# Kernel tuning notes

Hardware: AMD Instinct MI355X
Metric: run time of the kernel (lower is better)

Reference implementation:

```python
import jax, jax.numpy as jnp
import numpy as np

CL1_K = 25
CL2_K = 25


def cheb_stack(L, x0, K):
    # x0: (V, M) -> (K, V, M) Chebyshev basis T_k(L) x0
    if K == 1:
        return x0[None]
    x1 = L @ x0
    if K == 2:
        return jnp.stack([x0, x1])

    def step(carry, _):
        xm1, xm2 = carry
        xk = 2.0 * (L @ xm1) - xm2
        return (xk, xm1), xk

    _, rest = jax.lax.scan(step, (x1, x0), None, length=K - 2)
    return jnp.concatenate([x0[None], x1[None], rest], axis=0)


def graph_conv(x, L, W, b, K):
    # x: (B, C, V) -> (B, Fout, V); matches torch Graph_Conv permute/view logic
    B, C, V = x.shape
    x0 = x.transpose(2, 1, 0).reshape(V, C * B)
    xs = cheb_stack(L, x0, K)                              # (K, V, C*B)
    xs = xs.reshape(K, V, C, B).transpose(3, 1, 2, 0)      # (B, V, C, K)
    xs = xs.reshape(B * V, C * K)
    y = xs @ W.T + b                                       # (B*V, Fout)
    return y.reshape(B, V, -1).transpose(0, 2, 1)


def maxpool4(x):
    B, C, V = x.shape
    return x.reshape(B, C, V // 4, 4).max(axis=-1)


def setup_inputs() -> dict:
    key = jax.random.key(0)
    ks = jax.random.split(key, 10)
    B, C, V, Vp = 32, 16, 4000, 4096
    CL1_F, CL2_F, FC_F = 64, 128, 10
    x = jax.random.normal(ks[0], (B, C, V), dtype=jnp.float32)
    perm = jax.random.permutation(ks[1], Vp)
    # rescaled Laplacians, scaled for stable 25-step recurrence
    L1 = jax.random.normal(ks[2], (Vp, Vp), dtype=jnp.float32) * (0.3 / np.sqrt(Vp))
    L2 = jax.random.normal(ks[3], (Vp // 4, Vp // 4), dtype=jnp.float32) * (0.3 / np.sqrt(Vp // 4))
    W1 = jax.random.normal(ks[4], (CL1_F, C * CL1_K), dtype=jnp.float32) * np.sqrt(2.0 / (C * CL1_K + CL1_F))
    b1 = jnp.zeros((CL1_F,), dtype=jnp.float32)
    W2 = jax.random.normal(ks[5], (CL2_F, CL1_F * CL2_K), dtype=jnp.float32) * np.sqrt(2.0 / (CL1_F * CL2_K + CL2_F))
    b2 = jnp.zeros((CL2_F,), dtype=jnp.float32)
    FC_IN = CL2_F * Vp // 16
    Wfc = jax.random.normal(ks[6], (FC_F, FC_IN), dtype=jnp.float32) * np.sqrt(2.0 / (FC_IN + FC_F))
    bfc = jnp.zeros((FC_F,), dtype=jnp.float32)
    return {"x": x, "perm": perm, "L1": L1, "L2": L2, "W1": W1, "b1": b1,
            "W2": W2, "b2": b2, "Wfc": Wfc, "bfc": bfc}


def reference(x, perm, L1, L2, W1, b1, W2, b2, Wfc, bfc):
    # BatchNorm1d(affine=False), training-mode batch statistics
    mu = x.mean(axis=(0, 2), keepdims=True)
    var = x.var(axis=(0, 2), keepdims=True)
    x = (x - mu) / jnp.sqrt(var + 1e-5)
    # Permute: zero-pad vertices to len(perm), then index
    B, C, V = x.shape
    Vp = perm.shape[0]
    x = jnp.pad(x, ((0, 0), (0, 0), (0, Vp - V)))[:, :, perm]
    x = jax.nn.relu(graph_conv(x, L1, W1, b1, CL1_K))
    x = maxpool4(x)
    x = jax.nn.relu(graph_conv(x, L2, W2, b2, CL2_K))
    x = maxpool4(x)
    x = x.reshape(B, -1)
    # dropout in eval mode (identity)
    return x @ Wfc.T + bfc
```

## Files before the change

### kernel.cpp

```cpp
#include <hip/hip_runtime.h>

typedef _Float16 half8 __attribute__((ext_vector_type(8)));
typedef _Float16 half4 __attribute__((ext_vector_type(4)));
typedef float f32x4 __attribute__((ext_vector_type(4)));

__device__ __forceinline__ void gload_lds16(const void* g, void* l) {
  __builtin_amdgcn_global_load_lds((const __attribute__((address_space(1))) void*)g,
                                   (__attribute__((address_space(3))) void*)l, 16, 0, 0);
}

__global__ __launch_bounds__(256) void k_bn_partial(const float* __restrict__ x,
                                                    float* __restrict__ part) {
  const int c = blockIdx.x & 15;
  const int seg = blockIdx.x >> 4;
  const int t = threadIdx.x;
  float s = 0.f, s2 = 0.f;
  for (int b = 0; b < 32; ++b) {
    const float* row = x + (size_t)(b * 16 + c) * 4000 + seg * 500;
    for (int v = t; v < 500; v += 256) {
      float val = row[v];
      s += val;
      s2 += val * val;
    }
  }
#pragma unroll
  for (int off = 32; off > 0; off >>= 1) {
    s += __shfl_down(s, off);
    s2 += __shfl_down(s2, off);
  }
  __shared__ float rs_[4], rs2_[4];
  if ((t & 63) == 0) { rs_[t >> 6] = s; rs2_[t >> 6] = s2; }
  __syncthreads();
  if (t == 0) {
    part[c * 8 + seg] = rs_[0] + rs_[1] + rs_[2] + rs_[3];
    part[128 + c * 8 + seg] = rs2_[0] + rs2_[1] + rs2_[2] + rs2_[3];
  }
}

__global__ void k_bn_final(const float* __restrict__ part, float* __restrict__ musig) {
  const int c = threadIdx.x;
  if (c < 16) {
    float S = 0.f, S2 = 0.f;
#pragma unroll
    for (int seg = 0; seg < 8; ++seg) {
      S += part[c * 8 + seg];
      S2 += part[128 + c * 8 + seg];
    }
    const float inv = 1.f / 128000.f;
    float mu = S * inv;
    float var = S2 * inv - mu * mu;
    musig[c] = mu;
    musig[16 + c] = rsqrtf(var + 1e-5f);
  }
}

__global__ __launch_bounds__(256) void k_build_x0(const float* __restrict__ x,
                                                  const int* __restrict__ perm,
                                                  const float* __restrict__ musig,
                                                  _Float16* __restrict__ X0) {
  const int idx = blockIdx.x * 256 + threadIdx.x;
  const int v = idx & 4095;
  const int m = idx >> 12;
  const int b = m & 31;
  const int c = m >> 5;
  const int pv = perm[v];
  float val = 0.f;
  if (pv < 4000)
    val = (x[((size_t)(b * 16 + c)) * 4000 + pv] - musig[c]) * musig[16 + c] * 0.0625f;
  X0[idx] = (_Float16)val;
}

__global__ __launch_bounds__(256) void k_cvt_f16(const float* __restrict__ s,
                                                 _Float16* __restrict__ d, int n) {
  const int i = (blockIdx.x * 256 + threadIdx.x) * 4;
  if (i >= n) return;
  f32x4 v = *(const f32x4*)(s + i);
  half4 h;
  h[0] = (_Float16)v[0]; h[1] = (_Float16)v[1];
  h[2] = (_Float16)v[2]; h[3] = (_Float16)v[3];
  *(half4*)(d + i) = h;
}

__global__ __launch_bounds__(256) void k_prep_w(const float* __restrict__ W,
                                                _Float16* __restrict__ Wp,
                                                int F, int shiftC, int kround) {
  const int idx = blockIdx.x * 256 + threadIdx.x;
  const int CS = 1 << shiftC;
  const int KPtot = kround * CS;
  if (idx >= F * KPtot) return;
  const int f = idx / KPtot;
  const int rem = idx - f * KPtot;
  const int k = rem >> shiftC;
  const int c = rem & (CS - 1);
  float v = 0.f;
  if (k < 25) v = W[(size_t)f * (CS * 25) + c * 25 + k];
  Wp[idx] = (_Float16)v;
}

__global__ __launch_bounds__(512, 1) void k_cheb_ks(const _Float16* __restrict__ Xprev,
                                                    const _Float16* __restrict__ Lm,
                                                    _Float16* __restrict__ P) {
  __shared__ _Float16 lds[2][24576];
  const int t = threadIdx.x;
  const int lane = t & 63;
  const int w = t >> 6;
  const int wm = w >> 2, wn = w & 3;
  const int bid = blockIdx.x;
  const int bx = bid & 15;
  const int by = (bid >> 4) & 3;
  const int kq = bid >> 6;
  const int v0 = bx * 256, m0 = by * 128;
  const size_t rs = 8192;

  const char* Ag = (const char*)Xprev + (size_t)m0 * rs + (size_t)kq * 2048;
  const char* Bg = (const char*)Lm + (size_t)v0 * rs + (size_t)kq * 2048;
  const size_t soff = (size_t)(lane >> 3) * rs + (size_t)(((lane & 7) * 16) ^ ((lane >> 3) << 4));

  f32x4 acc[4][4] = {};

  auto stage = [&](int buf, int tt) {
    const char* ag = Ag + (size_t)tt * 128 + soff;
    const char* bg = Bg + (size_t)tt * 128 + soff;
    char* A = (char*)&lds[buf][0];
    char* B = (char*)&lds[buf][8192];
#pragma unroll
    for (int j = 0; j < 2; ++j) {
      const int r0 = w * 16 + j * 8;
      gload_lds16(ag + (size_t)r0 * rs, A + r0 * 128);
    }
#pragma unroll
    for (int j = 0; j < 4; ++j) {
      const int r0 = w * 32 + j * 8;
      gload_lds16(bg + (size_t)r0 * rs, B + r0 * 128);
    }
  };

  stage(0, 0);

  const int NT = 16;
  for (int tt = 0; tt < NT; ++tt) {
    const int cur = tt & 1;
    if (tt + 1 < NT) {
      stage(cur ^ 1, tt + 1);
      asm volatile("s_waitcnt vmcnt(6)" ::: "memory");
    } else {
      asm volatile("s_waitcnt vmcnt(0)" ::: "memory");
    }
    asm volatile("s_barrier" ::: "memory");
    const char* A = (const char*)&lds[cur][0];
    const char* B = (const char*)&lds[cur][8192];
#pragma unroll
    for (int kk = 0; kk < 2; ++kk) {
      const int cb = kk * 64 + ((lane >> 4) << 4);
      half8 a[4], b[4];
#pragma unroll
      for (int mi = 0; mi < 4; ++mi) {
        const int ar = wm * 64 + mi * 16 + (lane & 15);
        a[mi] = *(const half8*)(A + ar * 128 + (cb ^ ((ar & 7) << 4)));
      }
#pragma unroll
      for (int ni = 0; ni < 4; ++ni) {
        const int br = wn * 64 + ni * 16 + (lane & 15);
        b[ni] = *(const half8*)(B + br * 128 + (cb ^ ((br & 7) << 4)));
      }
#pragma unroll
      for (int mi = 0; mi < 4; ++mi)
#pragma unroll
        for (int ni = 0; ni < 4; ++ni)
          acc[mi][ni] = __builtin_amdgcn_mfma_f32_16x16x32_f16(a[mi], b[ni], acc[mi][ni], 0, 0, 0);
    }
    asm volatile("s_barrier" ::: "memory");
  }

  _Float16* Pq = P + (size_t)kq * 2097152;
  const int rbase = (lane >> 4) << 2;
#pragma unroll
  for (int mi = 0; mi < 4; ++mi) {
#pragma unroll
    for (int ni = 0; ni < 4; ++ni) {
      const int vv = v0 + wn * 64 + ni * 16 + (lane & 15);
#pragma unroll
      for (int r = 0; r < 4; ++r) {
        const int mm = m0 + wm * 64 + mi * 16 + rbase + r;
        Pq[(size_t)mm * 4096 + vv] = (_Float16)acc[mi][ni][r];
      }
    }
  }
}

__global__ __launch_bounds__(256) void k_cheb_red(const _Float16* __restrict__ P,
                                                  const _Float16* __restrict__ Xm2,
                                                  _Float16* __restrict__ Xout,
                                                  float alpha, float beta) {
  const int i = (blockIdx.x * 256 + threadIdx.x) * 8;
  half8 p0 = *(const half8*)(P + i);
  half8 p1 = *(const half8*)(P + 2097152 + i);
  half8 p2 = *(const half8*)(P + 4194304 + i);
  half8 p3 = *(const half8*)(P + 6291456 + i);
  half8 xm2 = {};
  if (beta != 0.f) xm2 = *(const half8*)(Xm2 + i);
  half8 o;
#pragma unroll
  for (int j = 0; j < 8; ++j) {
    float s = (float)p0[j] + (float)p1[j] + (float)p2[j] + (float)p3[j];
    o[j] = (_Float16)(alpha * s - beta * (float)xm2[j]);
  }
  *(half8*)(Xout + i) = o;
}

__global__ __launch_bounds__(512, 2) void k_cheb(const _Float16* __restrict__ Xprev,
                                                 const _Float16* __restrict__ Lm,
                                                 const _Float16* __restrict__ Xm2,
                                                 _Float16* __restrict__ Xout,
                                                 int V, float alpha, float beta) {
  __shared__ _Float16 lds[2][2][12288];
  const int t = threadIdx.x;
  const int lane = t & 63;
  const int w = t >> 6;
  const int kh = w >> 2;
  const int wl = w & 3;
  const int wr = wl >> 1, wc = wl & 1;
  const int v0 = blockIdx.x * 64;
  const int m0 = blockIdx.y * 128;
  const size_t rs = (size_t)V * 2;
  const int K2 = V >> 1;
  const int NT2 = K2 >> 6;

  const char* Ag = (const char*)Xprev + (size_t)m0 * rs + (size_t)kh * K2 * 2;
  const char* Bg = (const char*)Lm + (size_t)v0 * rs + (size_t)kh * K2 * 2;
  const size_t soff = (size_t)(lane >> 3) * rs + (size_t)(((lane & 7) * 16) ^ ((lane >> 3) << 4));

  f32x4 acc[4][2] = {};

  auto stage = [&](int buf, int tt) {
    const char* ag = Ag + (size_t)tt * 128 + soff;
    const char* bg = Bg + (size_t)tt * 128 + soff;
    char* A = (char*)&lds[kh][buf][0];
    char* B = (char*)&lds[kh][buf][8192];
#pragma unroll
    for (int j = 0; j < 4; ++j) {
      const int r0 = wl * 32 + j * 8;
      gload_lds16(ag + (size_t)r0 * rs, A + r0 * 128);
    }
#pragma unroll
    for (int j = 0; j < 2; ++j) {
      const int r0 = wl * 16 + j * 8;
      gload_lds16(bg + (size_t)r0 * rs, B + r0 * 128);
    }
  };

  stage(0, 0);

  for (int tt = 0; tt < NT2; ++tt) {
    const int cur = tt & 1;
    if (tt + 1 < NT2) {
      stage(cur ^ 1, tt + 1);
      asm volatile("s_waitcnt vmcnt(6)" ::: "memory");
    } else {
      asm volatile("s_waitcnt vmcnt(0)" ::: "memory");
    }
    asm volatile("s_barrier" ::: "memory");
    const char* A = (const char*)&lds[kh][cur][0];
    const char* B = (const char*)&lds[kh][cur][8192];
#pragma unroll
    for (int kk = 0; kk < 2; ++kk) {
      const int cb = kk * 64 + ((lane >> 4) << 4);
      half8 a[4], b[2];
#pragma unroll
      for (int mi = 0; mi < 4; ++mi) {
        const int ar = wr * 64 + mi * 16 + (lane & 15);
        a[mi] = *(const half8*)(A + ar * 128 + (cb ^ ((ar & 7) << 4)));
      }
#pragma unroll
      for (int ni = 0; ni < 2; ++ni) {
        const int br = wc * 32 + ni * 16 + (lane & 15);
        b[ni] = *(const half8*)(B + br * 128 + (cb ^ ((br & 7) << 4)));
      }
#pragma unroll
      for (int mi = 0; mi < 4; ++mi)
#pragma unroll
        for (int ni = 0; ni < 2; ++ni)
          acc[mi][ni] = __builtin_amdgcn_mfma_f32_16x16x32_f16(a[mi], b[ni], acc[mi][ni], 0, 0, 0);
    }
    asm volatile("s_barrier" ::: "memory");
  }

  __syncthreads();
  float* red = (float*)&lds[0][0][0];
  if (kh == 1) {
    float* dst = red + wl * 2048 + lane * 4;
#pragma unroll
    for (int mi = 0; mi < 4; ++mi)
#pragma unroll
      for (int ni = 0; ni < 2; ++ni)
        *(f32x4*)(dst + (mi * 2 + ni) * 256) = acc[mi][ni];
  }
  __syncthreads();
  if (kh == 0) {
    const float* src = red + wl * 2048 + lane * 4;
    const int rbase = (lane >> 4) << 2;
#pragma unroll
    for (int mi = 0; mi < 4; ++mi) {
#pragma unroll
      for (int ni = 0; ni < 2; ++ni) {
        f32x4 o = *(const f32x4*)(src + (mi * 2 + ni) * 256);
        const int vv = v0 + wc * 32 + ni * 16 + (lane & 15);
#pragma unroll
        for (int r = 0; r < 4; ++r) {
          const int mm = m0 + wr * 64 + mi * 16 + rbase + r;
          const size_t idx = (size_t)mm * V + vv;
          float val = alpha * (acc[mi][ni][r] + o[r]);
          if (beta != 0.f) val -= (float)Xm2[idx];
          Xout[idx] = (_Float16)val;
        }
      }
    }
  }
}

__global__ __launch_bounds__(256, 2) void k_dense(const _Float16* __restrict__ Wp,
                                                  const _Float16* __restrict__ XS,
                                                  const float* __restrict__ bias,
                                                  float* __restrict__ Yt,
                                                  int Vv, int shiftC, int nsteps,
                                                  size_t planeV, int Ntot,
                                                  float ascale, float bscale) {
  __shared__ _Float16 Alds[64 * 40];
  __shared__ _Float16 Blds[32 * 66];
  const int t = threadIdx.x;
  const int lane = t & 63;
  const int w = t >> 6;
  const int n0 = blockIdx.x * 64;
  const int f0 = blockIdx.y * 64;
  const int b = n0 / Vv;
  const int vb = n0 % Vv;
  const int KP = nsteps * 32;
  const int cmask = (1 << shiftC) - 1;

  f32x4 acc0 = {0.f, 0.f, 0.f, 0.f}, acc1 = {0.f, 0.f, 0.f, 0.f};
  f32x4 acc2 = {0.f, 0.f, 0.f, 0.f}, acc3 = {0.f, 0.f, 0.f, 0.f};

  for (int s = 0; s < nsteps; ++s) {
    const int q0 = s * 32;
    {
      const int row = t >> 2, cb = (t & 3) * 16;
      half8 v = *(const half8*)((const char*)Wp + ((size_t)(f0 + row) * KP + q0) * 2 + cb);
      *(half8*)((char*)Alds + row * 80 + cb) = v;
    }
    {
      const int q = q0 + (t >> 3), cb = (t & 7) * 16;
      const int k = q >> shiftC, c = q & cmask;
      half8 v = {};
      if (k < 25)
        v = *(const half8*)((const char*)XS +
                            ((size_t)k * planeV + (size_t)(c * 32 + b) * Vv + vb) * 2 + cb);
      uint4 uv = *(uint4*)&v;
      uint* ud = (uint*)((char*)Blds + (t >> 3) * 132 + cb);
      ud[0] = uv.x; ud[1] = uv.y; ud[2] = uv.z; ud[3] = uv.w;
    }
    __syncthreads();
    const int g16 = (lane >> 4) << 4;
    half8 a0 = *(const half8*)((char*)Alds + ((lane & 15) + 0) * 80 + g16);
    half8 a1 = *(const half8*)((char*)Alds + ((lane & 15) + 16) * 80 + g16);
    half8 a2 = *(const half8*)((char*)Alds + ((lane & 15) + 32) * 80 + g16);
    half8 a3 = *(const half8*)((char*)Alds + ((lane & 15) + 48) * 80 + g16);
    half8 bf;
    const int col = (w << 4) + (lane & 15);
#pragma unroll
    for (int j = 0; j < 8; ++j)
      bf[j] = Blds[(((lane >> 4) << 3) + j) * 66 + col];
    acc0 = __builtin_amdgcn_mfma_f32_16x16x32_f16(a0, bf, acc0, 0, 0, 0);
    acc1 = __builtin_amdgcn_mfma_f32_16x16x32_f16(a1, bf, acc1, 0, 0, 0);
    acc2 = __builtin_amdgcn_mfma_f32_16x16x32_f16(a2, bf, acc2, 0, 0, 0);
    acc3 = __builtin_amdgcn_mfma_f32_16x16x32_f16(a3, bf, acc3, 0, 0, 0);
    __syncthreads();
  }

  const int n = n0 + (w << 4) + (lane & 15);
  f32x4 accs[4] = {acc0, acc1, acc2, acc3};
#pragma unroll
  for (int mi = 0; mi < 4; ++mi) {
#pragma unroll
    for (int r = 0; r < 4; ++r) {
      const int f = f0 + (mi << 4) + ((lane >> 4) << 2) + r;
      float val = ascale * accs[mi][r] + bscale * bias[f];
      Yt[(size_t)f * Ntot + n] = fmaxf(val, 0.f);
    }
  }
}

__global__ __launch_bounds__(256) void k_pool1(const float* __restrict__ Yt,
                                               _Float16* __restrict__ X2) {
  const int idx = blockIdx.x * 256 + threadIdx.x;
  const int v2 = idx & 1023;
  const int rest = idx >> 10;
  const int b = rest & 31;
  const int f = rest >> 5;
  f32x4 q = *(const f32x4*)(Yt + (size_t)f * 131072 + b * 4096 + v2 * 4);
  float mx = fmaxf(fmaxf(q[0], q[1]), fmaxf(q[2], q[3]));
  X2[(size_t)(f * 32 + b) * 1024 + v2] = (_Float16)(mx * 0.015625f);
}

__global__ __launch_bounds__(256) void k_pool2(const float* __restrict__ Yt,
                                               float* __restrict__ p2) {
  const int idx = blockIdx.x * 256 + threadIdx.x;
  const int v3 = idx & 255;
  const int rest = idx >> 8;
  const int f = rest & 127;
  const int b = rest >> 7;
  f32x4 q = *(const f32x4*)(Yt + (size_t)f * 32768 + b * 1024 + v3 * 4);
  float mx = fmaxf(fmaxf(q[0], q[1]), fmaxf(q[2], q[3]));
  p2[(size_t)b * 32768 + f * 256 + v3] = mx;
}

__global__ __launch_bounds__(256) void k_fc_part(const float* __restrict__ p2,
                                                 const float* __restrict__ Wfc,
                                                 float* __restrict__ partF) {
  const int b = blockIdx.x >> 3;
  const int seg = blockIdx.x & 7;
  const int t = threadIdx.x;
  const int lane = t & 63;
  const int w = t >> 6;
  const int base = seg * 4096;
  float acc[10];
#pragma unroll
  for (int o = 0; o < 10; ++o) acc[o] = 0.f;
  const float* pb = p2 + (size_t)b * 32768 + base;
  for (int i = t; i < 4096; i += 256) {
    float p = pb[i];
#pragma unroll
    for (int o = 0; o < 10; ++o) acc[o] += p * Wfc[(size_t)o * 32768 + base + i];
  }
#pragma unroll
  for (int off = 32; off > 0; off >>= 1)
#pragma unroll
    for (int o = 0; o < 10; ++o) acc[o] += __shfl_down(acc[o], off);
  __shared__ float rws[10][4];
  if (lane == 0) {
#pragma unroll
    for (int o = 0; o < 10; ++o) rws[o][w] = acc[o];
  }
  __syncthreads();
  if (t < 10) partF[blockIdx.x * 10 + t] =
      rws[t][0] + rws[t][1] + rws[t][2] + rws[t][3];
}

__global__ void k_fc_final(const float* __restrict__ partF,
                           const float* __restrict__ bfc,
                           float* __restrict__ out) {
  const int t = threadIdx.x;
  if (t < 320) {
    const int b = t / 10, o = t - b * 10;
    float s = 0.f;
#pragma unroll
    for (int seg = 0; seg < 8; ++seg) s += partF[(b * 8 + seg) * 10 + o];
    out[b * 10 + o] = 64.f * s + bfc[o];
  }
}

extern "C" void kernel_launch(void* const* d_in, const int* in_sizes, int n_in,
                              void* d_out, int out_size, void* d_ws, size_t ws_size,
                              hipStream_t stream) {
  (void)in_sizes; (void)n_in; (void)out_size; (void)ws_size;
  const float* x = (const float*)d_in[0];
  const int* perm = (const int*)d_in[1];
  const float* L1 = (const float*)d_in[2];
  const float* L2 = (const float*)d_in[3];
  const float* W1 = (const float*)d_in[4];
  const float* b1 = (const float*)d_in[5];
  const float* W2 = (const float*)d_in[6];
  const float* b2 = (const float*)d_in[7];
  const float* Wfc = (const float*)d_in[8];
  const float* bfc = (const float*)d_in[9];
  float* out = (float*)d_out;

  char* ws = (char*)d_ws;
  size_t off = 0;
  auto alloc = [&](size_t bytes) {
    char* p = ws + off;
    off += (bytes + 255) & ~(size_t)255;
    return p;
  };
  _Float16* L1h = (_Float16*)alloc(16777216ull * 2);
  _Float16* L2h = (_Float16*)alloc(1048576ull * 2);
  _Float16* W1p = (_Float16*)alloc(64ull * 448 * 2);
  _Float16* W2p = (_Float16*)alloc(128ull * 1664 * 2);
  float* part = (float*)alloc(256 * 4);
  float* musig = (float*)alloc(32 * 4);
  float* partF = (float*)alloc(2560 * 4);
  _Float16* XS = (_Float16*)alloc(25ull * 2097152 * 2);
  _Float16* Pq = (_Float16*)alloc(4ull * 2097152 * 2);
  float* Yt = (float*)alloc(64ull * 131072 * 4);
  float* p2 = (float*)alloc(32ull * 128 * 256 * 4);

  k_cvt_f16<<<16384, 256, 0, stream>>>(L1, L1h, 16777216);
  k_cvt_f16<<<1024, 256, 0, stream>>>(L2, L2h, 1048576);
  k_prep_w<<<112, 256, 0, stream>>>(W1, W1p, 64, 4, 28);
  k_prep_w<<<832, 256, 0, stream>>>(W2, W2p, 128, 6, 26);
  k_bn_partial<<<128, 256, 0, stream>>>(x, part);
  k_bn_final<<<1, 64, 0, stream>>>(part, musig);
  k_build_x0<<<8192, 256, 0, stream>>>(x, perm, musig, XS);

  const size_t plane = 2097152;
  for (int k = 1; k < 25; ++k) {
    k_cheb_ks<<<256, 512, 0, stream>>>(XS + (size_t)(k - 1) * plane, L1h, Pq);
    k_cheb_red<<<1024, 256, 0, stream>>>(
        Pq, XS + (size_t)(k >= 2 ? k - 2 : 0) * plane, XS + (size_t)k * plane,
        (k == 1) ? 1.f : 2.f, (k == 1) ? 0.f : 1.f);
  }
  k_dense<<<dim3(2048, 1), 256, 0, stream>>>(W1p, XS, b1, Yt, 4096, 4, 14, plane,
                                             131072, 16.f, 1.f);
  k_pool1<<<8192, 256, 0, stream>>>(Yt, XS);
  for (int k = 1; k < 25; ++k) {
    k_cheb<<<dim3(16, 16), 512, 0, stream>>>(
        XS + (size_t)(k - 1) * plane, L2h,
        XS + (size_t)(k >= 2 ? k - 2 : 0) * plane, XS + (size_t)k * plane,
        1024, (k == 1) ? 1.f : 2.f, (k == 1) ? 0.f : 1.f);
  }
  k_dense<<<dim3(512, 2), 256, 0, stream>>>(W2p, XS, b2, Yt, 1024, 6, 52, plane,
                                            32768, 1.f, 0.015625f);
  k_pool2<<<4096, 256, 0, stream>>>(Yt, p2);
  k_fc_part<<<256, 256, 0, stream>>>(p2, Wfc, partF);
  k_fc_final<<<1, 320, 0, stream>>>(partF, bfc, out);
}
```

Baseline: 1.202 ms.

## Enlarge split-K Chebyshev tiles to 256x256 and double-buffer dense GEMM via LDS DMA

The layer-1 Chebyshev split-K GEMM moves from 128x256 tiles with 4 K-slices to 256x256 tiles with 8 K-slices, so the reduction kernel now sums 8 partials. The partials reuse the Yt buffer. The dense GEMM becomes a templated kernel that covers all output features in one block, with K-steps of 64 and double-buffered, swizzled LDS staged by direct global-to-LDS loads. Extra zeroed XS planes absorb the padded K reads, which removes the bounds checks. The larger tiles raise operand reuse and register pressure, and the wider split-K doubles the partial-sum traffic through the reduction kernel.

```diff
diff --git a/kernel.cpp b/kernel.cpp
--- a/kernel.cpp
+++ b/kernel.cpp
@@ -81,6 +81,11 @@
   *(half4*)(d + i) = h;
 }
 
+__global__ __launch_bounds__(256) void k_zero(_Float16* __restrict__ p, int n8) {
+  const int i = blockIdx.x * 256 + threadIdx.x;
+  if (i < n8) *(half8*)(p + (size_t)i * 8) = half8{};
+}
+
 __global__ __launch_bounds__(256) void k_prep_w(const float* __restrict__ W,
                                                 _Float16* __restrict__ Wp,
                                                 int F, int shiftC, int kround) {
@@ -100,62 +105,61 @@
 __global__ __launch_bounds__(512, 1) void k_cheb_ks(const _Float16* __restrict__ Xprev,
                                                     const _Float16* __restrict__ Lm,
                                                     _Float16* __restrict__ P) {
-  __shared__ _Float16 lds[2][24576];
+  __shared__ _Float16 lds[2][32768];
   const int t = threadIdx.x;
   const int lane = t & 63;
+  const int g = lane >> 4;
   const int w = t >> 6;
   const int wm = w >> 2, wn = w & 3;
   const int bid = blockIdx.x;
   const int bx = bid & 15;
-  const int by = (bid >> 4) & 3;
-  const int kq = bid >> 6;
-  const int v0 = bx * 256, m0 = by * 128;
+  const int kq = (bid >> 4) & 7;
+  const int by = bid >> 7;
+  const int v0 = bx * 256, m0 = by * 256;
   const size_t rs = 8192;
 
-  const char* Ag = (const char*)Xprev + (size_t)m0 * rs + (size_t)kq * 2048;
-  const char* Bg = (const char*)Lm + (size_t)v0 * rs + (size_t)kq * 2048;
-  const size_t soff = (size_t)(lane >> 3) * rs + (size_t)(((lane & 7) * 16) ^ ((lane >> 3) << 4));
-
-  f32x4 acc[4][4] = {};
+  const char* Ag = (const char*)Xprev + (size_t)m0 * rs + (size_t)kq * 1024;
+  const char* Bg = (const char*)Lm + (size_t)v0 * rs + (size_t)kq * 1024;
+
+  f32x4 acc[8][4] = {};
 
   auto stage = [&](int buf, int tt) {
-    const char* ag = Ag + (size_t)tt * 128 + soff;
-    const char* bg = Bg + (size_t)tt * 128 + soff;
     char* A = (char*)&lds[buf][0];
-    char* B = (char*)&lds[buf][8192];
-#pragma unroll
-    for (int j = 0; j < 2; ++j) {
-      const int r0 = w * 16 + j * 8;
-      gload_lds16(ag + (size_t)r0 * rs, A + r0 * 128);
-    }
+    char* B = (char*)&lds[buf][16384];
 #pragma unroll
     for (int j = 0; j < 4; ++j) {
-      const int r0 = w * 32 + j * 8;
-      gload_lds16(bg + (size_t)r0 * rs, B + r0 * 128);
+      const int ch = j * 512 + t;
+      const int row = ch >> 3, c8 = ch & 7;
+      gload_lds16(Ag + (size_t)row * rs + tt * 128 + ((c8 ^ (row & 7)) << 4), A + ch * 16);
+    }
+#pragma unroll
+    for (int j = 0; j < 4; ++j) {
+      const int ch = j * 512 + t;
+      const int row = ch >> 3, c8 = ch & 7;
+      gload_lds16(Bg + (size_t)row * rs + tt * 128 + ((c8 ^ (row & 7)) << 4), B + ch * 16);
     }
   };
 
   stage(0, 0);
 
-  const int NT = 16;
-  for (int tt = 0; tt < NT; ++tt) {
+  for (int tt = 0; tt < 8; ++tt) {
     const int cur = tt & 1;
-    if (tt + 1 < NT) {
+    if (tt + 1 < 8) {
       stage(cur ^ 1, tt + 1);
-      asm volatile("s_waitcnt vmcnt(6)" ::: "memory");
+      asm volatile("s_waitcnt vmcnt(8)" ::: "memory");
     } else {
       asm volatile("s_waitcnt vmcnt(0)" ::: "memory");
     }
     asm volatile("s_barrier" ::: "memory");
     const char* A = (const char*)&lds[cur][0];
-    const char* B = (const char*)&lds[cur][8192];
+    const char* B = (const char*)&lds[cur][16384];
 #pragma unroll
     for (int kk = 0; kk < 2; ++kk) {
-      const int cb = kk * 64 + ((lane >> 4) << 4);
-      half8 a[4], b[4];
-#pragma unroll
-      for (int mi = 0; mi < 4; ++mi) {
-        const int ar = wm * 64 + mi * 16 + (lane & 15);
+      const int cb = kk * 64 + (g << 4);
+      half8 a[8], b[4];
+#pragma unroll
+      for (int mi = 0; mi < 8; ++mi) {
+        const int ar = wm * 128 + mi * 16 + (lane & 15);
         a[mi] = *(const half8*)(A + ar * 128 + (cb ^ ((ar & 7) << 4)));
       }
 #pragma unroll
@@ -164,7 +168,7 @@
         b[ni] = *(const half8*)(B + br * 128 + (cb ^ ((br & 7) << 4)));
       }
 #pragma unroll
-      for (int mi = 0; mi < 4; ++mi)
+      for (int mi = 0; mi < 8; ++mi)
 #pragma unroll
         for (int ni = 0; ni < 4; ++ni)
           acc[mi][ni] = __builtin_amdgcn_mfma_f32_16x16x32_f16(a[mi], b[ni], acc[mi][ni], 0, 0, 0);
@@ -173,15 +177,15 @@
   }
 
   _Float16* Pq = P + (size_t)kq * 2097152;
-  const int rbase = (lane >> 4) << 2;
-#pragma unroll
-  for (int mi = 0; mi < 4; ++mi) {
+  const int rb = g << 2;
+#pragma unroll
+  for (int mi = 0; mi < 8; ++mi) {
 #pragma unroll
     for (int ni = 0; ni < 4; ++ni) {
       const int vv = v0 + wn * 64 + ni * 16 + (lane & 15);
 #pragma unroll
       for (int r = 0; r < 4; ++r) {
-        const int mm = m0 + wm * 64 + mi * 16 + rbase + r;
+        const int mm = m0 + wm * 128 + mi * 16 + rb + r;
         Pq[(size_t)mm * 4096 + vv] = (_Float16)acc[mi][ni][r];
       }
     }
@@ -192,19 +196,19 @@
                                                   const _Float16* __restrict__ Xm2,
                                                   _Float16* __restrict__ Xout,
                                                   float alpha, float beta) {
-  const int i = (blockIdx.x * 256 + threadIdx.x) * 8;
-  half8 p0 = *(const half8*)(P + i);
-  half8 p1 = *(const half8*)(P + 2097152 + i);
-  half8 p2 = *(const half8*)(P + 4194304 + i);
-  half8 p3 = *(const half8*)(P + 6291456 + i);
+  const size_t i = ((size_t)blockIdx.x * 256 + threadIdx.x) * 8;
+  float s[8] = {};
+#pragma unroll
+  for (int p = 0; p < 8; ++p) {
+    half8 v = *(const half8*)(P + (size_t)p * 2097152 + i);
+#pragma unroll
+    for (int j = 0; j < 8; ++j) s[j] += (float)v[j];
+  }
   half8 xm2 = {};
   if (beta != 0.f) xm2 = *(const half8*)(Xm2 + i);
   half8 o;
 #pragma unroll
-  for (int j = 0; j < 8; ++j) {
-    float s = (float)p0[j] + (float)p1[j] + (float)p2[j] + (float)p3[j];
-    o[j] = (_Float16)(alpha * s - beta * (float)xm2[j]);
-  }
+  for (int j = 0; j < 8; ++j) o[j] = (_Float16)(alpha * s[j] - beta * (float)xm2[j]);
   *(half8*)(Xout + i) = o;
 }
 
@@ -318,73 +322,97 @@
   }
 }
 
+template <int FT>
 __global__ __launch_bounds__(256, 2) void k_dense(const _Float16* __restrict__ Wp,
                                                   const _Float16* __restrict__ XS,
                                                   const float* __restrict__ bias,
                                                   float* __restrict__ Yt,
                                                   int Vv, int shiftC, int nsteps,
-                                                  size_t planeV, int Ntot,
-                                                  float ascale, float bscale) {
-  __shared__ _Float16 Alds[64 * 40];
-  __shared__ _Float16 Blds[32 * 66];
+                                                  int Ntot, float ascale, float bscale) {
+  __shared__ _Float16 Alds[2][FT * 64];
+  __shared__ _Float16 Blds[2][64 * 64];
   const int t = threadIdx.x;
   const int lane = t & 63;
+  const int g = lane >> 4;
   const int w = t >> 6;
   const int n0 = blockIdx.x * 64;
-  const int f0 = blockIdx.y * 64;
   const int b = n0 / Vv;
   const int vb = n0 % Vv;
-  const int KP = nsteps * 32;
+  const int Kp = nsteps * 64;
   const int cmask = (1 << shiftC) - 1;
-
-  f32x4 acc0 = {0.f, 0.f, 0.f, 0.f}, acc1 = {0.f, 0.f, 0.f, 0.f};
-  f32x4 acc2 = {0.f, 0.f, 0.f, 0.f}, acc3 = {0.f, 0.f, 0.f, 0.f};
+  const size_t plane = 2097152;
+
+  f32x4 acc[FT / 16] = {};
+
+  auto stage = [&](int buf, int s) {
+    const int q0 = s * 64;
+    char* A = (char*)&Alds[buf][0];
+    char* B = (char*)&Blds[buf][0];
+#pragma unroll
+    for (int j = 0; j < FT / 32; ++j) {
+      const int ch = j * 256 + t;
+      const int f = ch >> 3, c8 = ch & 7;
+      gload_lds16((const char*)Wp + ((size_t)f * Kp + q0) * 2 + ((c8 ^ (f & 7)) << 4),
+                  A + ch * 16);
+    }
+#pragma unroll
+    for (int j = 0; j < 2; ++j) {
+      const int ch = j * 256 + t;
+      const int q = ch >> 3, c8 = ch & 7;
+      const int qq = q0 + q;
+      const int k = qq >> shiftC, c = qq & cmask;
+      const int sz = (q >> 3) & 7;
+      gload_lds16((const char*)XS + ((size_t)k * plane + (size_t)(c * 32 + b) * Vv + vb) * 2 +
+                      ((c8 ^ sz) << 4),
+                  B + ch * 16);
+    }
+  };
+
+  stage(0, 0);
 
   for (int s = 0; s < nsteps; ++s) {
-    const int q0 = s * 32;
-    {
-      const int row = t >> 2, cb = (t & 3) * 16;
-      half8 v = *(const half8*)((const char*)Wp + ((size_t)(f0 + row) * KP + q0) * 2 + cb);
-      *(half8*)((char*)Alds + row * 80 + cb) = v;
-    }
-    {
-      const int q = q0 + (t >> 3), cb = (t & 7) * 16;
-      const int k = q >> shiftC, c = q & cmask;
-      half8 v = {};
-      if (k < 25)
-        v = *(const half8*)((const char*)XS +
-                            ((size_t)k * planeV + (size_t)(c * 32 + b) * Vv + vb) * 2 + cb);
-      uint4 uv = *(uint4*)&v;
-      uint* ud = (uint*)((char*)Blds + (t >> 3) * 132 + cb);
-      ud[0] = uv.x; ud[1] = uv.y; ud[2] = uv.z; ud[3] = uv.w;
-    }
-    __syncthreads();
-    const int g16 = (lane >> 4) << 4;
-    half8 a0 = *(const half8*)((char*)Alds + ((lane & 15) + 0) * 80 + g16);
-    half8 a1 = *(const half8*)((char*)Alds + ((lane & 15) + 16) * 80 + g16);
-    half8 a2 = *(const half8*)((char*)Alds + ((lane & 15) + 32) * 80 + g16);
-    half8 a3 = *(const half8*)((char*)Alds + ((lane & 15) + 48) * 80 + g16);
-    half8 bf;
-    const int col = (w << 4) + (lane & 15);
-#pragma unroll
-    for (int j = 0; j < 8; ++j)
-      bf[j] = Blds[(((lane >> 4) << 3) + j) * 66 + col];
-    acc0 = __builtin_amdgcn_mfma_f32_16x16x32_f16(a0, bf, acc0, 0, 0, 0);
-    acc1 = __builtin_amdgcn_mfma_f32_16x16x32_f16(a1, bf, acc1, 0, 0, 0);
-    acc2 = __builtin_amdgcn_mfma_f32_16x16x32_f16(a2, bf, acc2, 0, 0, 0);
-    acc3 = __builtin_amdgcn_mfma_f32_16x16x32_f16(a3, bf, acc3, 0, 0, 0);
-    __syncthreads();
-  }
-
-  const int n = n0 + (w << 4) + (lane & 15);
-  f32x4 accs[4] = {acc0, acc1, acc2, acc3};
-#pragma unroll
-  for (int mi = 0; mi < 4; ++mi) {
+    const int cur = s & 1;
+    if (s + 1 < nsteps) {
+      stage(cur ^ 1, s + 1);
+      if constexpr (FT == 64) {
+        asm volatile("s_waitcnt vmcnt(4)" ::: "memory");
+      } else {
+        asm volatile("s_waitcnt vmcnt(6)" ::: "memory");
+      }
+    } else {
+      asm volatile("s_waitcnt vmcnt(0)" ::: "memory");
+    }
+    asm volatile("s_barrier" ::: "memory");
+    const _Float16* A = &Alds[cur][0];
+    const _Float16* B = &Blds[cur][0];
+#pragma unroll
+    for (int kk = 0; kk < 2; ++kk) {
+      half8 bf;
+      const int c = lane & 15;
+#pragma unroll
+      for (int j = 0; j < 8; ++j) {
+        const int q = kk * 32 + g * 8 + j;
+        const int sz = (q >> 3) & 7;
+        bf[j] = B[q * 64 + ((w * 16 + c) ^ (sz << 3))];
+      }
+#pragma unroll
+      for (int mi = 0; mi < FT / 16; ++mi) {
+        const int ar = mi * 16 + c;
+        half8 af = *(const half8*)((const char*)A + ar * 128 +
+                                   ((kk * 64 + g * 16) ^ ((ar & 7) << 4)));
+        acc[mi] = __builtin_amdgcn_mfma_f32_16x16x32_f16(af, bf, acc[mi], 0, 0, 0);
+      }
+    }
+    asm volatile("s_barrier" ::: "memory");
+  }
+
+  const int n = n0 + w * 16 + (lane & 15);
+#pragma unroll
+  for (int mi = 0; mi < FT / 16; ++mi) {
 #pragma unroll
     for (int r = 0; r < 4; ++r) {
-      const int f = f0 + (mi << 4) + ((lane >> 4) << 2) + r;
-      float val = ascale * accs[mi][r] + bscale * bias[f];
-      Yt[(size_t)f * Ntot + n] = fmaxf(val, 0.f);
+      const int f = mi * 16 + g * 4 + r;
+      Yt[(size_t)f * Ntot + n] = fmaxf(ascale * acc[mi][r] + bscale * bias[f], 0.f);
     }
   }
 }
@@ -488,28 +516,30 @@
   float* part = (float*)alloc(256 * 4);
   float* musig = (float*)alloc(32 * 4);
   float* partF = (float*)alloc(2560 * 4);
-  _Float16* XS = (_Float16*)alloc(25ull * 2097152 * 2);
-  _Float16* Pq = (_Float16*)alloc(4ull * 2097152 * 2);
+  _Float16* XS = (_Float16*)alloc(28ull * 2097152 * 2);
   float* Yt = (float*)alloc(64ull * 131072 * 4);
   float* p2 = (float*)alloc(32ull * 128 * 256 * 4);
+  _Float16* Pq = (_Float16*)Yt;
+
+  const size_t plane = 2097152;
 
   k_cvt_f16<<<16384, 256, 0, stream>>>(L1, L1h, 16777216);
   k_cvt_f16<<<1024, 256, 0, stream>>>(L2, L2h, 1048576);
   k_prep_w<<<112, 256, 0, stream>>>(W1, W1p, 64, 4, 28);
   k_prep_w<<<832, 256, 0, stream>>>(W2, W2p, 128, 6, 26);
+  k_zero<<<3072, 256, 0, stream>>>(XS + 25 * plane, 786432);
   k_bn_partial<<<128, 256, 0, stream>>>(x, part);
   k_bn_final<<<1, 64, 0, stream>>>(part, musig);
   k_build_x0<<<8192, 256, 0, stream>>>(x, perm, musig, XS);
 
-  const size_t plane = 2097152;
   for (int k = 1; k < 25; ++k) {
     k_cheb_ks<<<256, 512, 0, stream>>>(XS + (size_t)(k - 1) * plane, L1h, Pq);
     k_cheb_red<<<1024, 256, 0, stream>>>(
         Pq, XS + (size_t)(k >= 2 ? k - 2 : 0) * plane, XS + (size_t)k * plane,
         (k == 1) ? 1.f : 2.f, (k == 1) ? 0.f : 1.f);
   }
-  k_dense<<<dim3(2048, 1), 256, 0, stream>>>(W1p, XS, b1, Yt, 4096, 4, 14, plane,
-                                             131072, 16.f, 1.f);
+  k_dense<64><<<dim3(2048, 1), 256, 0, stream>>>(W1p, XS, b1, Yt, 4096, 4, 7,
+                                                 131072, 16.f, 1.f);
   k_pool1<<<8192, 256, 0, stream>>>(Yt, XS);
   for (int k = 1; k < 25; ++k) {
     k_cheb<<<dim3(16, 16), 512, 0, stream>>>(
@@ -517,8 +547,8 @@
         XS + (size_t)(k >= 2 ? k - 2 : 0) * plane, XS + (size_t)k * plane,
         1024, (k == 1) ? 1.f : 2.f, (k == 1) ? 0.f : 1.f);
   }
-  k_dense<<<dim3(512, 2), 256, 0, stream>>>(W2p, XS, b2, Yt, 1024, 6, 52, plane,
-                                            32768, 1.f, 0.015625f);
+  k_dense<128><<<dim3(512, 1), 256, 0, stream>>>(W2p, XS, b2, Yt, 1024, 6, 26,
+                                                 32768, 1.f, 0.015625f);
   k_pool2<<<4096, 256, 0, stream>>>(Yt, p2);
   k_fc_part<<<256, 256, 0, stream>>>(p2, Wfc, partF);
   k_fc_final<<<1, 320, 0, stream>>>(partF, bfc, out);
```

After: 1.283 ms. 6.7% more time.
